# Optimization experiments

Hardware: AMD Instinct MI355X
Metric: run time of the kernel (lower is better)

Reference implementation:

```python
import jax, jax.numpy as jnp
import numpy as np

B = 8192
N_SUP = 4
N_EXH = 4
N_OUTER = 50      # solver default; torch loop breaks early on tol/stall, replicated via done mask
N_INNER = 15
TOL = 1e-3
DESIGN_PRESSURE = 500.0
DESIGN_FLOW = 2.0
MAX_PRESSURE = 800.0
MOTOR_EFF = 0.9


def setup_inputs() -> dict:
    key = jax.random.key(0)
    k1, k2, k3 = jax.random.split(key, 3)
    fan_speed = 0.5 + 0.5 * jax.random.uniform(k1, (B,), dtype=jnp.float32)
    supply_damper_pos = 0.2 + 0.8 * jax.random.uniform(k2, (B, N_SUP), dtype=jnp.float32)
    exhaust_damper_pos = 0.2 + 0.8 * jax.random.uniform(k3, (B, N_EXH), dtype=jnp.float32)
    # FanModel.__init__ parameter init
    max_flow = DESIGN_FLOW * 1.3
    a_init = MAX_PRESSURE * 1000.0
    c_init = -MAX_PRESSURE * 1000.0 / max_flow ** 2
    b_init = (DESIGN_PRESSURE - a_init - c_init * DESIGN_FLOW ** 2) / DESIGN_FLOW
    fan_a = jnp.asarray(a_init / 1000.0, jnp.float32)
    fan_b = jnp.asarray(b_init, jnp.float32)
    fan_c = jnp.asarray(c_init, jnp.float32)
    # BranchModel / DamperModel parameter init (vectorized over branches)
    def branch_params(n):
        return (jnp.full((n,), np.log(50.0), jnp.float32),            # log_R_duct
                jnp.full((n,), 5.0, jnp.float32),                     # R_linear
                jnp.full((n,), np.log(10.0), jnp.float32),            # damper log_R_open
                jnp.full((n,), np.log(100000.0 / 10.0), jnp.float32)) # damper k
    slr, srl, sdo, sdk = branch_params(N_SUP)
    elr, erl, edo, edk = branch_params(N_EXH)
    return {
        'fan_speed': fan_speed,
        'supply_damper_pos': supply_damper_pos,
        'exhaust_damper_pos': exhaust_damper_pos,
        'fan_a': fan_a, 'fan_b': fan_b, 'fan_c': fan_c,
        'sup_log_R_duct': slr, 'sup_R_linear': srl, 'sup_damp_log_R_open': sdo, 'sup_damp_k': sdk,
        'exh_log_R_duct': elr, 'exh_R_linear': erl, 'exh_damp_log_R_open': edo, 'exh_damp_k': edk,
    }


def _branch_dp(flow, pos, log_R_duct, R_linear, damp_log_R_open, damp_k):
    # flow, pos: [B, n]; params: [n]; flow_exponent == 2.0
    aq = jnp.abs(flow)
    dp_duct = jnp.exp(log_R_duct) * aq ** 2 + jnp.abs(R_linear) * aq
    R_damp = jnp.exp(damp_log_R_open) * jnp.exp(damp_k * (1.0 - pos))
    return dp_duct + R_damp * aq ** 2


def _distribute(total_flow, pos, bp):
    n = pos.shape[1]
    flows = jnp.broadcast_to(total_flow[:, None] / n, pos.shape)
    for _ in range(N_INNER):
        p = _branch_dp(flows, pos, *bp)
        target = p.mean(axis=1, keepdims=True)
        R_eq = p / (flows ** 2 + 1e-6)
        new = jnp.sqrt(jnp.clip(target / (R_eq + 1e-6), 0.0, None))
        flows = new * total_flow[:, None] / (new.sum(axis=1, keepdims=True) + 1e-6)
    return flows, _branch_dp(flows, pos, *bp)


def _fan_pressure(flow, speed, a, b, c):
    fn = flow / (speed + 1e-6)
    pd = a * 1000.0 + b * fn + c * fn ** 2
    return jnp.maximum(pd * speed ** 2, 0.0)


def _forward(fan_speed, supply_damper_pos, exhaust_damper_pos, fan_a, fan_b, fan_c,
             sup_bp, exh_bp):
    def system_pressure(flow):
        _, sp = _distribute(flow, supply_damper_pos, sup_bp)
        _, ep = _distribute(flow, exhaust_damper_pos, exh_bp)
        return sp[:, 0] + ep[:, 0]

    flow_scale = DESIGN_FLOW / (DESIGN_PRESSURE + 1e-6)

    def step(carry, i):
        flow, prev_err, stall, done = carry
        res = _fan_pressure(flow, fan_speed, fan_a, fan_b, fan_c) - system_pressure(flow)
        err = jnp.max(jnp.abs(res))
        stalled = jnp.abs(err - prev_err) < 1e-6
        stall = jnp.where(stalled, stall + 1, 0)
        done = done | (err < TOL) | (stall > 10)
        alpha = jnp.maximum(0.5 * 0.95 ** i, 0.05)
        flow_new = jnp.clip(flow + alpha * res * flow_scale, 0.01, DESIGN_FLOW * 1.5)
        flow = jnp.where(done, flow, flow_new)
        prev_err = jnp.where(done, prev_err, err)
        return (flow, prev_err, stall, done), None

    init = (fan_speed * DESIGN_FLOW,
            jnp.asarray(jnp.inf, jnp.float32),
            jnp.asarray(0, jnp.int32),
            jnp.asarray(False))
    (flow, _, _, _), _ = jax.lax.scan(step, init, jnp.arange(N_OUTER, dtype=jnp.float32))

    flow = jnp.maximum(flow, 0.0)
    fan_p = _fan_pressure(flow, fan_speed, fan_a, fan_b, fan_c)
    sys_p = system_pressure(flow)
    # FanModel.get_power
    fr = flow / (DESIGN_FLOW + 1e-6)
    pr = fan_p / (DESIGN_PRESSURE + 1e-6)
    eta = jnp.clip(0.65 * (1.0 - 0.3 * (fr - 1.0) ** 2 - 0.2 * (pr - 1.0) ** 2), 0.3, 0.75)
    power = flow * fan_p / (eta * MOTOR_EFF + 1e-6)
    sf, sp = _distribute(flow, supply_damper_pos, sup_bp)
    ef, ep = _distribute(flow, exhaust_damper_pos, exh_bp)
    # pack dict outputs into one [B, 4 + 2*N_SUP + 2*N_EXH] array
    return jnp.concatenate([flow[:, None], fan_p[:, None], sys_p[:, None], power[:, None],
                            sf, sp, ef, ep], axis=1)


def reference(fan_speed, supply_damper_pos, exhaust_damper_pos, fan_a, fan_b, fan_c,
              sup_log_R_duct, sup_R_linear, sup_damp_log_R_open, sup_damp_k,
              exh_log_R_duct, exh_R_linear, exh_damp_log_R_open, exh_damp_k):
    sup_bp = (sup_log_R_duct, sup_R_linear, sup_damp_log_R_open, sup_damp_k)
    exh_bp = (exh_log_R_duct, exh_R_linear, exh_damp_log_R_open, exh_damp_k)
    return _forward(fan_speed, supply_damper_pos, exhaust_damper_pos,
                    fan_a, fan_b, fan_c, sup_bp, exh_bp)
```

## Files before the change

### kernel.cpp

```cpp
#include <hip/hip_runtime.h>
#include <math.h>

#define BATCH   8192
#define NOUTER  50
#define NINNER  15
#define NTHREADS (BATCH * 8)

__device__ __forceinline__ float fast_rcp(float x)  { return __builtin_amdgcn_rcpf(x); }
__device__ __forceinline__ float fast_sqrt(float x) { return __builtin_amdgcn_sqrtf(x); }

template <int CTRL>
__device__ __forceinline__ float dpp_movf(float x) {
    return __int_as_float(__builtin_amdgcn_update_dpp(
        0, __float_as_int(x), CTRL, 0xF, 0xF, true));
}
#define DPP_XOR1  0xB1
#define DPP_XOR2  0x4E
#define DPP_BQ0   0x00
#define DPP_ROR8  0x128
#define DPP_HMIR  0x141

__device__ __forceinline__ float distribute_lane(float total, float R2, float Rl,
                                                 float& pout) {
    float f = total * 0.25f;
#pragma unroll
    for (int it = 0; it < NINNER; ++it) {
        float p  = fmaf(R2, f * f, Rl * f);
        float t  = p + dpp_movf<DPP_XOR1>(p);
        t       += dpp_movf<DPP_XOR2>(t);
        float target = t * 0.25f;
        float q2e = fmaf(f, f, 1e-6f);
        float den = fmaf(q2e, 1e-6f, p);
        float ratio = target * q2e * fast_rcp(den);
        float nw = fast_sqrt(ratio);
        float s  = nw + dpp_movf<DPP_XOR1>(nw);
        s       += dpp_movf<DPP_XOR2>(s);
        f = nw * total * fast_rcp(s + 1e-6f);
    }
    pout = fmaf(R2, f * f, Rl * f);
    return f;
}

__device__ __forceinline__ float fan_pressure(float flow, float rspeed, float speed2,
                                              float a1000, float b, float c) {
    float fn = flow * rspeed;
    float pd = fmaf(c, fn * fn, fmaf(b, fn, a1000));
    return fmaxf(pd * speed2, 0.0f);
}

__device__ __forceinline__ float sys_from_p(float pfin) {
    float p0 = dpp_movf<DPP_BQ0>(pfin);
    return p0 + dpp_movf<DPP_HMIR>(p0);
}

struct LaneConsts {
    float R2, Rl;
    float speed, rspeed, speed2, a1000, b, c;
    int elem, lane, sub;
};

__device__ __forceinline__ LaneConsts setup_lane(
        const float* fan_speed,
        const float* sup_pos, const float* exh_pos,
        const float* pa, const float* pb, const float* pc,
        const float* slr, const float* srl, const float* sdo, const float* sdk,
        const float* elr, const float* erl, const float* edo, const float* edk) {
    LaneConsts L;
    int t   = blockIdx.x * blockDim.x + threadIdx.x;
    L.elem  = t >> 3;
    L.sub   = t & 7;
    int net = (L.sub >> 2) & 1;
    int j   = L.sub & 3;
    L.lane  = threadIdx.x & 63;

    const float* pos = net ? exh_pos : sup_pos;
    const float* lr  = net ? elr : slr;
    const float* rl  = net ? erl : srl;
    const float* dlo = net ? edo : sdo;
    const float* dk  = net ? edk : sdk;

    float Rduct = expf(lr[j]);
    float Rd    = expf(dlo[j]) * expf(dk[j] * (1.0f - pos[L.elem * 4 + j]));
    L.R2 = Rduct + Rd;
    L.Rl = fabsf(rl[j]);

    L.speed  = fan_speed[L.elem];
    L.rspeed = fast_rcp(L.speed + 1e-6f);
    L.speed2 = L.speed * L.speed;
    L.a1000  = pa[0] * 1000.0f;
    L.b      = pb[0];
    L.c      = pc[0];
    return L;
}

__global__ __launch_bounds__(256) void phase1(
        const float* __restrict__ fan_speed,
        const float* __restrict__ sup_pos, const float* __restrict__ exh_pos,
        const float* __restrict__ pa, const float* __restrict__ pb, const float* __restrict__ pc,
        const float* __restrict__ slr, const float* __restrict__ srl,
        const float* __restrict__ sdo, const float* __restrict__ sdk,
        const float* __restrict__ elr, const float* __restrict__ erl,
        const float* __restrict__ edo, const float* __restrict__ edk,
        float* __restrict__ slots, float* __restrict__ hist,
        float* __restrict__ stage, int use_hist) {
    LaneConsts L = setup_lane(fan_speed, sup_pos, exh_pos, pa, pb, pc,
                              slr, srl, sdo, sdk, elr, erl, edo, edk);
    int t = blockIdx.x * blockDim.x + threadIdx.x;
    const float flow_scale = 2.0f / (500.0f + 1e-6f);
    float flow = L.speed * 2.0f;
    float alpha_base = 0.5f;

#pragma unroll 1
    for (int i = 0; i < NOUTER; ++i) {
        float pfin;
        (void)distribute_lane(flow, L.R2, L.Rl, pfin);
        float sys  = sys_from_p(pfin);
        float res  = fan_pressure(flow, L.rspeed, L.speed2, L.a1000, L.b, L.c) - sys;
        float ares = fabsf(res);

        if (stage) {
            stage[(size_t)i * NTHREADS + t] = ares;
        } else {
            float m = ares;
            m = fmaxf(m, dpp_movf<DPP_ROR8>(m));
            m = fmaxf(m, __shfl_xor(m, 16));
            m = fmaxf(m, __shfl_xor(m, 32));
            if (L.lane == 0)
                atomicMax((int*)&slots[i], __float_as_int(m));
        }

        float alpha = fmaxf(alpha_base, 0.05f);
        alpha_base *= 0.95f;
        float fnew = fmaf(alpha * res, flow_scale, flow);
        flow = fminf(fmaxf(fnew, 0.01f), 3.0f);
        if (use_hist && L.sub == 0) hist[(size_t)i * BATCH + L.elem] = flow;
    }
}

__global__ __launch_bounds__(1024) void phase1b(const float* __restrict__ stage,
                                                float* __restrict__ slots) {
    const float4* src = (const float4*)(stage + (size_t)blockIdx.x * NTHREADS);
    float m = 0.0f;
#pragma unroll 4
    for (int k = threadIdx.x; k < NTHREADS / 4; k += 1024) {
        float4 v = src[k];
        m = fmaxf(m, fmaxf(fmaxf(v.x, v.y), fmaxf(v.z, v.w)));
    }
#pragma unroll
    for (int off = 32; off; off >>= 1) m = fmaxf(m, __shfl_xor(m, off));
    __shared__ float red[16];
    if ((threadIdx.x & 63) == 0) red[threadIdx.x >> 6] = m;
    __syncthreads();
    if (threadIdx.x == 0) {
        float v = red[0];
#pragma unroll
        for (int i = 1; i < 16; ++i) v = fmaxf(v, red[i]);
        slots[blockIdx.x] = v;
    }
}

template <bool USE_HIST>
__global__ __launch_bounds__(256) void phase3(
        const float* __restrict__ fan_speed,
        const float* __restrict__ sup_pos, const float* __restrict__ exh_pos,
        const float* __restrict__ pa, const float* __restrict__ pb, const float* __restrict__ pc,
        const float* __restrict__ slr, const float* __restrict__ srl,
        const float* __restrict__ sdo, const float* __restrict__ sdk,
        const float* __restrict__ elr, const float* __restrict__ erl,
        const float* __restrict__ edo, const float* __restrict__ edk,
        const float* __restrict__ slots, const float* __restrict__ hist,
        float* __restrict__ out) {
    LaneConsts L = setup_lane(fan_speed, sup_pos, exh_pos, pa, pb, pc,
                              slr, srl, sdo, sdk, elr, erl, edo, edk);

    float prev = INFINITY;
    int stall = 0, k = NOUTER;
    bool done = false;
#pragma unroll 1
    for (int i = 0; i < NOUTER; ++i) {
        float err = slots[i];
        bool stalled = fabsf(err - prev) < 1e-6f;
        stall = stalled ? stall + 1 : 0;
        done = done || (err < 1e-3f) || (stall > 10);
        if (done) { k = i; break; }
        prev = err;
    }

    const float flow_scale = 2.0f / (500.0f + 1e-6f);
    float flow;
    if (USE_HIST) {
        flow = (k == 0) ? L.speed * 2.0f : hist[(size_t)(k - 1) * BATCH + L.elem];
    } else {
        flow = L.speed * 2.0f;
        float alpha_base = 0.5f;
#pragma unroll 1
        for (int i = 0; i < k; ++i) {
            float pfin;
            (void)distribute_lane(flow, L.R2, L.Rl, pfin);
            float sys = sys_from_p(pfin);
            float res = fan_pressure(flow, L.rspeed, L.speed2, L.a1000, L.b, L.c) - sys;
            float alpha = fmaxf(alpha_base, 0.05f);
            alpha_base *= 0.95f;
            float fnew = fmaf(alpha * res, flow_scale, flow);
            flow = fminf(fmaxf(fnew, 0.01f), 3.0f);
        }
    }

    flow = fmaxf(flow, 0.0f);
    float fanp = fan_pressure(flow, L.rspeed, L.speed2, L.a1000, L.b, L.c);

    float pfin;
    float ffin = distribute_lane(flow, L.R2, L.Rl, pfin);
    float sys  = sys_from_p(pfin);

    float fr  = flow * (1.0f / (2.0f + 1e-6f));
    float pr  = fanp * (1.0f / (500.0f + 1e-6f));
    float eta = 0.65f * (1.0f - 0.3f * (fr - 1.0f) * (fr - 1.0f)
                              - 0.2f * (pr - 1.0f) * (pr - 1.0f));
    eta = fminf(fmaxf(eta, 0.3f), 0.75f);
    float power = flow * fanp * fast_rcp(eta * 0.9f + 1e-6f);

    float* o = out + (size_t)L.elem * 20;
    if (L.sub == 0) {
        o[0] = flow; o[1] = fanp; o[2] = sys; o[3] = power;
    }
    int net = (L.sub >> 2) & 1;
    int j   = L.sub & 3;
    o[4 + net * 8 + j] = ffin;
    o[8 + net * 8 + j] = pfin;
}

extern "C" void kernel_launch(void* const* d_in, const int* in_sizes, int n_in,
                              void* d_out, int out_size, void* d_ws, size_t ws_size,
                              hipStream_t stream) {
    const float* fan_speed = (const float*)d_in[0];
    const float* sup_pos   = (const float*)d_in[1];
    const float* exh_pos   = (const float*)d_in[2];
    const float* pa        = (const float*)d_in[3];
    const float* pb        = (const float*)d_in[4];
    const float* pc        = (const float*)d_in[5];
    const float* slr       = (const float*)d_in[6];
    const float* srl       = (const float*)d_in[7];
    const float* sdo       = (const float*)d_in[8];
    const float* sdk       = (const float*)d_in[9];
    const float* elr       = (const float*)d_in[10];
    const float* erl       = (const float*)d_in[11];
    const float* edo       = (const float*)d_in[12];
    const float* edk       = (const float*)d_in[13];

    float* ws    = (float*)d_ws;
    float* slots = ws;
    float* hist  = ws + 64;
    float* stage = ws + 64 + BATCH * NOUTER;

    size_t need_hist  = (size_t)(64 + BATCH * NOUTER) * sizeof(float);
    size_t need_stage = need_hist + (size_t)NOUTER * NTHREADS * sizeof(float);
    bool use_hist  = ws_size >= need_hist;
    bool use_stage = ws_size >= need_stage;

    dim3 grid(NTHREADS / 256), block(256);

    phase1<<<grid, block, 0, stream>>>(fan_speed, sup_pos, exh_pos, pa, pb, pc,
                                       slr, srl, sdo, sdk, elr, erl, edo, edk,
                                       slots, hist, use_stage ? stage : nullptr,
                                       use_hist ? 1 : 0);
    if (use_stage)
        phase1b<<<dim3(NOUTER), dim3(1024), 0, stream>>>(stage, slots);

    if (use_hist) {
        phase3<true><<<grid, block, 0, stream>>>(fan_speed, sup_pos, exh_pos, pa, pb, pc,
                                                 slr, srl, sdo, sdk, elr, erl, edo, edk,
                                                 slots, hist, (float*)d_out);
    } else {
        phase3<false><<<grid, block, 0, stream>>>(fan_speed, sup_pos, exh_pos, pa, pb, pc,
                                                  slr, srl, sdo, sdk, elr, erl, edo, edk,
                                                  slots, nullptr, (float*)d_out);
    }
}
```

Baseline: 138.1 us.

## Reduce residual max per wave in phase1 and compute stop index once

Phase1 now reduces |residual| across each wave with DPP row broadcasts and stores one value per wave, not one per thread. This shrinks the staging buffer from NOUTER*NTHREADS floats to NOUTER*NWAVES. Phase1b becomes a single block that reduces the per-wave maxima, runs the convergence/stall logic once, and writes the stop index k. Phase3 then reads k instead of having every thread scan the slots. The cost is a few extra DPP ops per outer iteration and a serial single-block reduction kernel.

```diff
diff --git a/kernel.cpp b/kernel.cpp
--- a/kernel.cpp
+++ b/kernel.cpp
@@ -5,6 +5,7 @@
 #define NOUTER  50
 #define NINNER  15
 #define NTHREADS (BATCH * 8)
+#define NWAVES  (NTHREADS / 64)
 
 __device__ __forceinline__ float fast_rcp(float x)  { return __builtin_amdgcn_rcpf(x); }
 __device__ __forceinline__ float fast_sqrt(float x) { return __builtin_amdgcn_sqrtf(x); }
@@ -19,6 +20,8 @@
 #define DPP_BQ0   0x00
 #define DPP_ROR8  0x128
 #define DPP_HMIR  0x141
+#define DPP_BC15  0x142
+#define DPP_BC31  0x143
 
 __device__ __forceinline__ float distribute_lane(float total, float R2, float Rl,
                                                  float& pout) {
@@ -106,6 +109,7 @@
     LaneConsts L = setup_lane(fan_speed, sup_pos, exh_pos, pa, pb, pc,
                               slr, srl, sdo, sdk, elr, erl, edo, edk);
     int t = blockIdx.x * blockDim.x + threadIdx.x;
+    int wave = t >> 6;
     const float flow_scale = 2.0f / (500.0f + 1e-6f);
     float flow = L.speed * 2.0f;
     float alpha_base = 0.5f;
@@ -119,7 +123,11 @@
         float ares = fabsf(res);
 
         if (stage) {
-            stage[(size_t)i * NTHREADS + t] = ares;
+            float m = fmaxf(ares, dpp_movf<DPP_ROR8>(ares));
+            m = fmaxf(m, dpp_movf<DPP_BC15>(m));
+            m = fmaxf(m, dpp_movf<DPP_BC31>(m));
+            if (L.lane == 63)
+                stage[i * NWAVES + wave] = m;
         } else {
             float m = ares;
             m = fmaxf(m, dpp_movf<DPP_ROR8>(m));
@@ -138,24 +146,38 @@
 }
 
 __global__ __launch_bounds__(1024) void phase1b(const float* __restrict__ stage,
-                                                float* __restrict__ slots) {
-    const float4* src = (const float4*)(stage + (size_t)blockIdx.x * NTHREADS);
-    float m = 0.0f;
-#pragma unroll 4
-    for (int k = threadIdx.x; k < NTHREADS / 4; k += 1024) {
-        float4 v = src[k];
-        m = fmaxf(m, fmaxf(fmaxf(v.x, v.y), fmaxf(v.z, v.w)));
-    }
+                                                int* __restrict__ kout) {
+    __shared__ float sl[NOUTER];
+    int lane = threadIdx.x & 63;
+    int wv   = threadIdx.x >> 6;
+#pragma unroll 1
+    for (int i = wv; i < NOUTER; i += 16) {
+        const float4* src = (const float4*)(stage + (size_t)i * NWAVES);
+        float m = 0.0f;
 #pragma unroll
-    for (int off = 32; off; off >>= 1) m = fmaxf(m, __shfl_xor(m, off));
-    __shared__ float red[16];
-    if ((threadIdx.x & 63) == 0) red[threadIdx.x >> 6] = m;
+        for (int q = 0; q < 4; ++q) {
+            float4 v = src[lane + 64 * q];
+            m = fmaxf(m, fmaxf(fmaxf(v.x, v.y), fmaxf(v.z, v.w)));
+        }
+#pragma unroll
+        for (int off = 32; off; off >>= 1) m = fmaxf(m, __shfl_xor(m, off));
+        if (lane == 0) sl[i] = m;
+    }
     __syncthreads();
     if (threadIdx.x == 0) {
-        float v = red[0];
-#pragma unroll
-        for (int i = 1; i < 16; ++i) v = fmaxf(v, red[i]);
-        slots[blockIdx.x] = v;
+        float prev = INFINITY;
+        int stall = 0, k = NOUTER;
+        bool done = false;
+#pragma unroll 1
+        for (int i = 0; i < NOUTER; ++i) {
+            float err = sl[i];
+            bool stalled = fabsf(err - prev) < 1e-6f;
+            stall = stalled ? stall + 1 : 0;
+            done = done || (err < 1e-3f) || (stall > 10);
+            if (done) { k = i; break; }
+            prev = err;
+        }
+        *kout = k;
     }
 }
 
@@ -168,22 +190,27 @@
         const float* __restrict__ sdo, const float* __restrict__ sdk,
         const float* __restrict__ elr, const float* __restrict__ erl,
         const float* __restrict__ edo, const float* __restrict__ edk,
-        const float* __restrict__ slots, const float* __restrict__ hist,
-        float* __restrict__ out) {
+        const float* __restrict__ slots, const int* __restrict__ kin, int use_k,
+        const float* __restrict__ hist, float* __restrict__ out) {
     LaneConsts L = setup_lane(fan_speed, sup_pos, exh_pos, pa, pb, pc,
                               slr, srl, sdo, sdk, elr, erl, edo, edk);
 
-    float prev = INFINITY;
-    int stall = 0, k = NOUTER;
-    bool done = false;
-#pragma unroll 1
-    for (int i = 0; i < NOUTER; ++i) {
-        float err = slots[i];
-        bool stalled = fabsf(err - prev) < 1e-6f;
-        stall = stalled ? stall + 1 : 0;
-        done = done || (err < 1e-3f) || (stall > 10);
-        if (done) { k = i; break; }
-        prev = err;
+    int k;
+    if (use_k) {
+        k = *kin;
+    } else {
+        float prev = INFINITY;
+        int stall = 0; k = NOUTER;
+        bool done = false;
+#pragma unroll 1
+        for (int i = 0; i < NOUTER; ++i) {
+            float err = slots[i];
+            bool stalled = fabsf(err - prev) < 1e-6f;
+            stall = stalled ? stall + 1 : 0;
+            done = done || (err < 1e-3f) || (stall > 10);
+            if (done) { k = i; break; }
+            prev = err;
+        }
     }
 
     const float flow_scale = 2.0f / (500.0f + 1e-6f);
@@ -250,11 +277,12 @@
 
     float* ws    = (float*)d_ws;
     float* slots = ws;
-    float* hist  = ws + 64;
-    float* stage = ws + 64 + BATCH * NOUTER;
-
-    size_t need_hist  = (size_t)(64 + BATCH * NOUTER) * sizeof(float);
-    size_t need_stage = need_hist + (size_t)NOUTER * NTHREADS * sizeof(float);
+    int*   kptr  = (int*)(ws + 64);
+    float* hist  = ws + 128;
+    float* stage = ws + 128 + BATCH * NOUTER;
+
+    size_t need_hist  = (size_t)(128 + BATCH * NOUTER) * sizeof(float);
+    size_t need_stage = need_hist + (size_t)NOUTER * NWAVES * sizeof(float);
     bool use_hist  = ws_size >= need_hist;
     bool use_stage = ws_size >= need_stage;
 
@@ -265,15 +293,17 @@
                                        slots, hist, use_stage ? stage : nullptr,
                                        use_hist ? 1 : 0);
     if (use_stage)
-        phase1b<<<dim3(NOUTER), dim3(1024), 0, stream>>>(stage, slots);
+        phase1b<<<dim3(1), dim3(1024), 0, stream>>>(stage, kptr);
 
     if (use_hist) {
         phase3<true><<<grid, block, 0, stream>>>(fan_speed, sup_pos, exh_pos, pa, pb, pc,
                                                  slr, srl, sdo, sdk, elr, erl, edo, edk,
-                                                 slots, hist, (float*)d_out);
+                                                 slots, kptr, use_stage ? 1 : 0,
+                                                 hist, (float*)d_out);
     } else {
         phase3<false><<<grid, block, 0, stream>>>(fan_speed, sup_pos, exh_pos, pa, pb, pc,
                                                   slr, srl, sdo, sdk, elr, erl, edo, edk,
-                                                  slots, nullptr, (float*)d_out);
-    }
-}
+                                                  slots, kptr, use_stage ? 1 : 0,
+                                                  nullptr, (float*)d_out);
+    }
+}
```

New measurement: 134.0 us. 1.03x faster.
